# Kernel tuning notes

Measured on AMD Instinct MI355X. Metric: run time of the kernel, lower is better.

## Reference

```python
import jax, jax.numpy as jnp
import numpy as np

TEMP = 0.07
MOMENTUM = 0.2
K = 8192          # number of sampled negatives per row
NUM_CLASSES = 1000
B, N, D = 256, 32768, 2048
NEG_INF = -1e30


def _gumbel(key, shape):
    u = jax.random.uniform(key, shape, minval=1e-6, maxval=1.0)
    return -jnp.log(-jnp.log(u))


def setup_inputs() -> dict:
    key = jax.random.key(0)
    k1, k2, k3, k4, k5 = jax.random.split(key, 5)
    f = jax.random.normal(k1, (B, D), dtype=jnp.float32)
    f_nv = jax.random.normal(k2, (B, D), dtype=jnp.float32)
    # warmed-up memory bank (the real module L2-normalizes rows on update)
    features = jax.random.normal(k3, (N, D), dtype=jnp.float32)
    features = features / jnp.linalg.norm(features, axis=1, keepdims=True)
    labels = jax.random.randint(k4, (N,), 0, NUM_CLASSES)
    indexes = jax.random.randint(k5, (B,), 0, N)
    return {"f": f, "f_nv": f_nv, "features": features,
            "labels": labels, "indexes": indexes}


def reference(f, f_nv, features, labels, indexes):
    rkey = jax.random.key(42)
    kg1, kg2, kg3 = jax.random.split(rkey, 3)
    k = features                                   # [N, D] memory bank snapshot
    bsz = f.shape[0]

    # l_pos = <f_nv_i, k[indexes_i]>
    l_pos = jnp.sum(f_nv * k[indexes], axis=1, keepdims=True)   # [B, 1]

    mat = jnp.matmul(f, k.T)                       # [B, N]
    mat_sim = jnp.matmul(f_nv, k.T)                # [B, N]

    batch_labels = labels[indexes]                 # [B]
    pos_mask = labels[None, :] == batch_labels[:, None]         # [B, N]

    # torch.randperm-based sampling -> vectorized masked Gumbel sampling.
    # argmax of gumbel restricted to mask = uniform draw from masked set;
    # top-K of gumbel restricted to complement = K draws w/o replacement.
    g1 = _gumbel(kg1, (bsz, k.shape[0]))
    g2 = _gumbel(kg2, (bsz, k.shape[0]))
    g3 = _gumbel(kg3, (bsz, k.shape[0]))

    pos_idx_wogan = jnp.argmax(jnp.where(pos_mask, g1, NEG_INF), axis=1)
    positives_wogan = jnp.take_along_axis(mat, pos_idx_wogan[:, None], axis=1)  # [B,1]

    pos_idx = jnp.argmax(jnp.where(pos_mask, g2, NEG_INF), axis=1)
    positives = jnp.take_along_axis(mat_sim, pos_idx[:, None], axis=1)          # [B,1]

    _, neg_idx = jax.lax.top_k(jnp.where(pos_mask, NEG_INF, g3), K)             # [B,K]
    negatives = jnp.take_along_axis(mat_sim, neg_idx, axis=1)                   # [B,K]

    def ce_target0(logits):
        # CrossEntropyLoss with all targets == 0
        return -jax.nn.log_softmax(logits, axis=1)[:, 0].mean()

    self_out = jnp.concatenate([l_pos, negatives], axis=1) / TEMP
    inter_out = jnp.concatenate([positives, negatives], axis=1) / TEMP
    inter_out_wogan = jnp.concatenate([positives_wogan, negatives], axis=1) / TEMP

    memory_loss = ce_target0(self_out) + ce_target0(inter_out) + ce_target0(inter_out_wogan)

    # no-grad momentum update of the bank (F.normalize uses eps=1e-12)
    upd = MOMENTUM * k[indexes] + (1.0 - MOMENTUM) * f
    upd = upd / jnp.maximum(jnp.linalg.norm(upd, axis=1, keepdims=True), 1e-12)
    new_features = jax.lax.stop_gradient(features.at[indexes].set(upd))

    return memory_loss, new_features
```

## Files before the change

kernel.cpp:

```cpp
#include <hip/hip_runtime.h>
#include <stdint.h>

#define TEMP      0.07f
#define BATCH     256
#define NROWS     32768
#define DIM       2048
#define KNEG      8192

typedef __attribute__((ext_vector_type(8))) short bf16x8;
typedef __attribute__((ext_vector_type(4))) float f32x4;

__host__ __device__ inline void tf2x32(uint32_t ka, uint32_t kb,
                                       uint32_t x0, uint32_t x1,
                                       uint32_t& o0, uint32_t& o1) {
  uint32_t ks2 = ka ^ kb ^ 0x1BD11BDAu;
#define TFR(r) { x0 += x1; x1 = (x1 << r) | (x1 >> (32 - r)); x1 ^= x0; }
  x0 += ka; x1 += kb;
  TFR(13) TFR(15) TFR(26) TFR(6)
  x0 += kb;  x1 += ks2 + 1u;
  TFR(17) TFR(29) TFR(16) TFR(24)
  x0 += ks2; x1 += ka + 2u;
  TFR(13) TFR(15) TFR(26) TFR(6)
  x0 += ka;  x1 += kb + 3u;
  TFR(17) TFR(29) TFR(16) TFR(24)
  x0 += kb;  x1 += ks2 + 4u;
  TFR(13) TFR(15) TFR(26) TFR(6)
  x0 += ks2; x1 += ka + 5u;
#undef TFR
  o0 = x0; o1 = x1;
}

__device__ inline uint32_t ubits_at(uint32_t ka, uint32_t kb, uint32_t q) {
  uint32_t a, b; tf2x32(ka, kb, 0u, q, a, b);
  return (a ^ b) >> 9;
}

__device__ inline float block_sum(float v, float* sm) {
  __syncthreads();
  const int lane = threadIdx.x & 63;
  const int w = threadIdx.x >> 6;
  const int nw = blockDim.x >> 6;
  for (int o = 32; o; o >>= 1) v += __shfl_down(v, o, 64);
  if (lane == 0) sm[w] = v;
  __syncthreads();
  if (w == 0) {
    float x = (lane < nw) ? sm[lane] : 0.f;
    for (int o = 8; o; o >>= 1) x += __shfl_down(x, o, 64);
    if (lane == 0) sm[0] = x;
  }
  __syncthreads();
  return sm[0];
}

#define BM 256
#define BN 128
#define BK 64
#define NT (DIM / BK)

__device__ inline uint32_t pk2(float a, float b) {
  uint32_t ua = __float_as_uint(a), ub = __float_as_uint(b);
  ua = (ua + 0x7FFFu + ((ua >> 16) & 1u)) >> 16;
  ub = (ub + 0x7FFFu + ((ub >> 16) & 1u)) >> 16;
  return ua | (ub << 16);
}

__global__ __launch_bounds__(512, 2) void gemm_fused(
    const float* __restrict__ A,
    const float* __restrict__ B,
    float* __restrict__ C,
    float* __restrict__ outF,
    int copy_skip_rows) {
  __shared__ short As[2][BM * BK];
  __shared__ short Bs[2][BN * BK];
  const int t = threadIdx.x;
  const int bn = blockIdx.x;
  const int lane = t & 63, wave = t >> 6;
  const int wr = wave >> 2, wc = wave & 3;
  const int ld_row = t >> 4;
  const int ld_c4 = t & 15;

  float4 ra[8], rb[4];
  f32x4 acc[8][2] = {};

#define LOADT(k0)                                                              \
  {                                                                            \
    _Pragma("unroll")                                                          \
    for (int s = 0; s < 8; ++s)                                                \
      ra[s] = *(const float4*)&A[(size_t)(ld_row + 32 * s) * DIM + (k0) + ld_c4 * 4]; \
    _Pragma("unroll")                                                          \
    for (int s = 0; s < 4; ++s)                                                \
      rb[s] = *(const float4*)&B[(size_t)(bn * BN + ld_row + 32 * s) * DIM + (k0) + ld_c4 * 4]; \
  }

#define WRITET(buf, k0)                                                        \
  {                                                                            \
    _Pragma("unroll")                                                          \
    for (int s = 0; s < 8; ++s) {                                              \
      int r = ld_row + 32 * s;                                                 \
      uint32_t off = (uint32_t)r * (BK * 2) +                                  \
                     (((uint32_t)ld_c4 * 8) ^ (((uint32_t)r & 7u) << 4));      \
      *(uint2*)((char*)As[buf] + off) =                                        \
          make_uint2(pk2(ra[s].x, ra[s].y), pk2(ra[s].z, ra[s].w));            \
    }                                                                          \
    _Pragma("unroll")                                                          \
    for (int s = 0; s < 4; ++s) {                                              \
      int r = ld_row + 32 * s;                                                 \
      uint32_t off = (uint32_t)r * (BK * 2) +                                  \
                     (((uint32_t)ld_c4 * 8) ^ (((uint32_t)r & 7u) << 4));      \
      *(uint2*)((char*)Bs[buf] + off) =                                        \
          make_uint2(pk2(rb[s].x, rb[s].y), pk2(rb[s].z, rb[s].w));            \
      int g = bn * BN + r;                                                     \
      if (g >= copy_skip_rows) {                                               \
        float* d = &outF[(size_t)g * DIM + (k0) + ld_c4 * 4];                  \
        d[0] = rb[s].x; d[1] = rb[s].y; d[2] = rb[s].z; d[3] = rb[s].w;        \
      }                                                                        \
    }                                                                          \
  }

#define COMPUTET(buf)                                                          \
  {                                                                            \
    _Pragma("unroll")                                                          \
    for (int kk = 0; kk < 2; ++kk) {                                           \
      bf16x8 af[8], bfr[2];                                                    \
      const uint32_t kb = (uint32_t)(kk * 64 + ((lane >> 4) << 4));            \
      _Pragma("unroll")                                                        \
      for (int m = 0; m < 8; ++m) {                                            \
        uint32_t rr = (uint32_t)(wr * 128 + m * 16 + (lane & 15));             \
        af[m] = *(const bf16x8*)((const char*)As[buf] + rr * (BK * 2) +        \
                                 (kb ^ ((rr & 7u) << 4)));                     \
      }                                                                        \
      _Pragma("unroll")                                                        \
      for (int n = 0; n < 2; ++n) {                                            \
        uint32_t rr = (uint32_t)(wc * 32 + n * 16 + (lane & 15));              \
        bfr[n] = *(const bf16x8*)((const char*)Bs[buf] + rr * (BK * 2) +       \
                                  (kb ^ ((rr & 7u) << 4)));                    \
      }                                                                        \
      _Pragma("unroll")                                                        \
      for (int m = 0; m < 8; ++m)                                              \
        _Pragma("unroll")                                                      \
        for (int n = 0; n < 2; ++n)                                            \
          acc[m][n] = __builtin_amdgcn_mfma_f32_16x16x32_bf16(                 \
              af[m], bfr[n], acc[m][n], 0, 0, 0);                              \
    }                                                                          \
  }

  LOADT(0);
  WRITET(0, 0);
  __syncthreads();
  for (int t0 = 0; t0 < NT; ++t0) {
    if (t0 + 1 < NT) LOADT((t0 + 1) * BK);
    COMPUTET(t0 & 1);
    if (t0 + 1 < NT) {
      WRITET((t0 + 1) & 1, (t0 + 1) * BK);
      __syncthreads();
    }
  }

  const int col_l = lane & 15, rg = (lane >> 4) * 4;
#pragma unroll
  for (int m = 0; m < 8; ++m)
#pragma unroll
    for (int n = 0; n < 2; ++n) {
      size_t base = (size_t)(wr * 128 + m * 16 + rg) * NROWS
                  + (size_t)(bn * BN + wc * 32 + n * 16 + col_l);
#pragma unroll
      for (int r = 0; r < 4; ++r)
        C[base + (size_t)r * NROWS] = acc[m][n][r];
    }
#undef LOADT
#undef WRITET
#undef COMPUTET
}

__global__ __launch_bounds__(1024) void sample_loss(
    const float* __restrict__ f, const float* __restrict__ f_nv,
    const float* __restrict__ features, const int* __restrict__ labels,
    const int* __restrict__ indexes, const float* __restrict__ mat_sim,
    float* __restrict__ row_loss,
    uint32_t k1a, uint32_t k1b, uint32_t k2a, uint32_t k2b,
    uint32_t k3a, uint32_t k3b) {
  __shared__ uint32_t keys[NROWS];
  __shared__ uint32_t hist4[4][256];
  __shared__ uint32_t hist[256];
  __shared__ unsigned long long am1, am2;
  __shared__ int tie_j[128];
  __shared__ int tie_cnt;
  __shared__ float sred[16];
  __shared__ float swm[16], sws[16];
  __shared__ uint32_t bc_prefix, bc_rem;
  __shared__ int blab_s;

  const int t = threadIdx.x;
  const int i = blockIdx.x;
  const size_t mbase = (size_t)i * NROWS;

  if (t == 0) {
    blab_s = labels[indexes[i]];
    am1 = 0ull; am2 = 0ull; tie_cnt = 0;
  }
  __syncthreads();
  const int blab = blab_s;

#pragma unroll 2
  for (int s = 0; s < NROWS / 1024; ++s) {
    int j = t + 1024 * s;
    uint32_t q = (uint32_t)i * NROWS + (uint32_t)j;
    int lab = labels[j];
    if (lab == blab) {
      keys[j] = 0u;
      unsigned long long lo = (unsigned long long)(uint32_t)(NROWS - 1 - j);
      uint32_t u1 = ubits_at(k1a, k1b, q);
      uint32_t u2 = ubits_at(k2a, k2b, q);
      atomicMax(&am1, ((unsigned long long)u1 << 32) | lo);
      atomicMax(&am2, ((unsigned long long)u2 << 32) | lo);
    } else {
      keys[j] = ubits_at(k3a, k3b, q);
    }
  }
  __syncthreads();

  const int jw = NROWS - 1 - (int)(unsigned)(am1 & 0xFFFFFFFFull);
  const int jp = NROWS - 1 - (int)(unsigned)(am2 & 0xFFFFFFFFull);

  const int bank = indexes[i];
  float d1 = 0.f, d2 = 0.f, d3 = 0.f;
  for (int d = t; d < DIM; d += 1024) {
    float fnv = f_nv[(size_t)i * DIM + d];
    d1 += fnv * features[(size_t)bank * DIM + d];
    d2 += f[(size_t)i * DIM + d] * features[(size_t)jw * DIM + d];
    d3 += fnv * features[(size_t)jp * DIM + d];
  }
  const float l_pos = block_sum(d1, sred);
  const float posw  = block_sum(d2, sred);
  const float posv  = block_sum(d3, sred);

  uint32_t prefix = 0, remaining = KNEG;
  const int shifts[3] = {15, 7, 0};
  const int nbits[3]  = {8, 8, 7};
  for (int p = 0; p < 3; ++p) {
    const int sh = shifts[p];
    const int nb = 1 << nbits[p];
    ((uint32_t*)hist4)[t] = 0u;
    __syncthreads();
    const int hsel = t >> 8;
    for (int s = 0; s < NROWS / 1024; ++s) {
      int j = t + 1024 * s;
      uint32_t k = keys[j];
      bool ok = (p == 0) || ((k >> (sh + nbits[p])) == prefix);
      if (ok) atomicAdd(&hist4[hsel][(k >> sh) & (uint32_t)(nb - 1)], 1u);
    }
    __syncthreads();
    if (t < nb) hist[t] = hist4[0][t] + hist4[1][t] + hist4[2][t] + hist4[3][t];
    __syncthreads();
    if (t == 0) {
      uint32_t c = 0; int b = nb - 1;
      for (;; --b) {
        c += hist[b];
        if (c >= remaining || b == 0) break;
      }
      bc_prefix = (prefix << nbits[p]) | (uint32_t)b;
      bc_rem = remaining - (c - hist[b]);
    }
    __syncthreads();
    prefix = bc_prefix; remaining = bc_rem;
  }
  const uint32_t T = prefix;
  const uint32_t need = remaining;

  float m = -INFINITY, ssum = 0.f;
  for (int s = 0; s < NROWS / 1024; ++s) {
    int j = t + 1024 * s;
    uint32_t k = keys[j];
    if (k > T) {
      float v = mat_sim[mbase + j] / TEMP;
      if (v <= m) ssum += expf(v - m);
      else { ssum = ssum * expf(m - v) + 1.0f; m = v; }
    } else if (k == T) {
      int p = atomicAdd(&tie_cnt, 1);
      if (p < 128) tie_j[p] = j;
    }
  }
  for (int o = 32; o; o >>= 1) {
    float m2 = __shfl_down(m, o, 64);
    float s2 = __shfl_down(ssum, o, 64);
    if (m2 > m) { ssum = ssum * expf(m - m2) + s2; m = m2; }
    else if (m2 != -INFINITY) ssum += s2 * expf(m2 - m);
  }
  if ((t & 63) == 0) { swm[t >> 6] = m; sws[t >> 6] = ssum; }
  __syncthreads();
  if (t < 64) {
    float mm = (t < 16) ? swm[t] : -INFINITY;
    float ss = (t < 16) ? sws[t] : 0.f;
    for (int o = 8; o; o >>= 1) {
      float m2 = __shfl_down(mm, o, 64);
      float s2 = __shfl_down(ss, o, 64);
      if (m2 > mm) { ss = ss * expf(mm - m2) + s2; mm = m2; }
      else if (m2 != -INFINITY) ss += s2 * expf(m2 - mm);
    }
    if (t == 0) { swm[0] = mm; sws[0] = ss; }
  }
  __syncthreads();

  if (t == 0) {
    float M = swm[0], S = sws[0];
    int tc = tie_cnt;
    if (tc <= 128) {
      for (int a2 = 1; a2 < tc; ++a2) {
        int v = tie_j[a2]; int b2 = a2 - 1;
        while (b2 >= 0 && tie_j[b2] > v) { tie_j[b2 + 1] = tie_j[b2]; --b2; }
        tie_j[b2 + 1] = v;
      }
      for (uint32_t r = 0; r < need; ++r) {
        float v = mat_sim[mbase + tie_j[r]] / TEMP;
        if (v <= M) S += expf(v - M);
        else { S = S * expf(M - v) + 1.0f; M = v; }
      }
    } else {
      uint32_t taken = 0;
      for (int j = 0; j < NROWS && taken < need; ++j) {
        if (keys[j] == T) {
          float v = mat_sim[mbase + j] / TEMP;
          if (v <= M) S += expf(v - M);
          else { S = S * expf(M - v) + 1.0f; M = v; }
          ++taken;
        }
      }
    }
    float lp = l_pos / TEMP, pv = posv / TEMP, pw = posw / TEMP;
    float L = 0.f;
    { float X = fmaxf(M, lp); L += X + logf(expf(lp - X) + S * expf(M - X)) - lp; }
    { float X = fmaxf(M, pv); L += X + logf(expf(pv - X) + S * expf(M - X)) - pv; }
    { float X = fmaxf(M, pw); L += X + logf(expf(pw - X) + S * expf(M - X)) - pw; }
    row_loss[i] = L;
  }
}

__global__ void finalize_loss(const float* __restrict__ row_loss,
                              float* __restrict__ out) {
  __shared__ float sm[4];
  int t = threadIdx.x;
  float v = row_loss[t];
  for (int o = 32; o; o >>= 1) v += __shfl_down(v, o, 64);
  if ((t & 63) == 0) sm[t >> 6] = v;
  __syncthreads();
  if (t == 0) out[0] = (sm[0] + sm[1] + sm[2] + sm[3]) * (1.0f / BATCH);
}

__global__ void copy_front(const float* __restrict__ src,
                           float* __restrict__ dst, int n4) {
  int idx = blockIdx.x * blockDim.x + threadIdx.x;
  int stride = gridDim.x * blockDim.x;
  for (int i = idx; i < n4; i += stride) {
    float4 v = *(const float4*)&src[(size_t)i * 4];
    float* d = &dst[(size_t)i * 4];
    d[0] = v.x; d[1] = v.y; d[2] = v.z; d[3] = v.w;
  }
}

__global__ __launch_bounds__(256) void update_rows(
    const float* __restrict__ f, const float* __restrict__ features,
    const int* __restrict__ indexes, float* __restrict__ outF) {
  __shared__ float sred[16];
  const int i = blockIdx.x;
  const int row = indexes[i];
  for (int i2 = i + 1; i2 < BATCH; ++i2)
    if (indexes[i2] == row) return;
  const int t = threadIdx.x;
  float ss = 0.f;
  for (int d = t; d < DIM; d += 256) {
    float u = 0.2f * features[(size_t)row * DIM + d] + 0.8f * f[(size_t)i * DIM + d];
    ss += u * u;
  }
  ss = block_sum(ss, sred);
  float nrm = fmaxf(sqrtf(ss), 1e-12f);
  for (int d = t; d < DIM; d += 256) {
    float u = 0.2f * features[(size_t)row * DIM + d] + 0.8f * f[(size_t)i * DIM + d];
    outF[(size_t)row * DIM + d] = u / nrm;
  }
}

extern "C" void kernel_launch(void* const* d_in, const int* in_sizes, int n_in,
                              void* d_out, int out_size, void* d_ws, size_t ws_size,
                              hipStream_t stream) {
  (void)in_sizes; (void)n_in; (void)out_size;
  const float* f        = (const float*)d_in[0];
  const float* f_nv     = (const float*)d_in[1];
  const float* features = (const float*)d_in[2];
  const int*   labels   = (const int*)d_in[3];
  const int*   indexes  = (const int*)d_in[4];
  float* out = (float*)d_out;

  const size_t need = ((size_t)BATCH * NROWS + 256) * sizeof(float);
  float* mat_sim;
  float* row_loss;
  int skip_rows;
  bool use_ws = (d_ws != nullptr) && (ws_size >= need);
  if (use_ws) {
    mat_sim = (float*)d_ws;
    row_loss = mat_sim + (size_t)BATCH * NROWS;
    skip_rows = 0;
  } else {
    mat_sim = out + 4;
    row_loss = out + 4 + (size_t)BATCH * NROWS;
    skip_rows = 4224;
  }

  uint32_t c[6];
  { uint32_t a, b;
    tf2x32(0u, 42u, 0u, 0u, a, b); c[0] = a; c[1] = b;
    tf2x32(0u, 42u, 0u, 1u, a, b); c[2] = a; c[3] = b;
    tf2x32(0u, 42u, 0u, 2u, a, b); c[4] = a; c[5] = b; }

  gemm_fused<<<dim3(NROWS / BN), dim3(512), 0, stream>>>(
      f_nv, features, mat_sim, out + 1, skip_rows);
  sample_loss<<<dim3(BATCH), dim3(1024), 0, stream>>>(
      f, f_nv, features, labels, indexes, mat_sim, row_loss,
      c[0], c[1], c[2], c[3], c[4], c[5]);
  finalize_loss<<<dim3(1), dim3(256), 0, stream>>>(row_loss, out);
  if (!use_ws) {
    copy_front<<<dim3(2048), dim3(256), 0, stream>>>(
        features, out + 1, 4224 * DIM / 4);
  }
  update_rows<<<dim3(BATCH), dim3(256), 0, stream>>>(f, features, indexes, out + 1);
}
```

Measured before the change: 289.0 us.

## Pre-convert A to MFMA-fragment bf16 layout and shrink GEMM column tiles

A new kernel converts f_nv to bf16 once and stores it in the exact per-lane MFMA fragment order. The GEMM then reads A fragments straight from global memory (mostly cache hits) and keeps only B in shared memory. Column tiles shrink from 128 to 32 with 256 threads, which raises the block count and occupancy. The aim is to remove the redundant per-block fp32-to-bf16 conversion and LDS staging of A. In exchange, A fragments are re-read from L2 by every block, and the fallback path moves the copy skip boundary to make room for the new buffer.

After: 299.4 us. 1.04x slower.

```diff
diff --git a/kernel.cpp b/kernel.cpp
--- a/kernel.cpp
+++ b/kernel.cpp
@@ -52,11 +52,6 @@
   return sm[0];
 }
 
-#define BM 256
-#define BN 128
-#define BK 64
-#define NT (DIM / BK)
-
 __device__ inline uint32_t pk2(float a, float b) {
   uint32_t ua = __float_as_uint(a), ub = __float_as_uint(b);
   ua = (ua + 0x7FFFu + ((ua >> 16) & 1u)) >> 16;
@@ -64,112 +59,105 @@
   return ua | (ub << 16);
 }
 
-__global__ __launch_bounds__(512, 2) void gemm_fused(
-    const float* __restrict__ A,
+__global__ __launch_bounds__(256) void cvtA(const float* __restrict__ A,
+                                            uint32_t* __restrict__ Abf) {
+  const int t = threadIdx.x;
+  const int w = blockIdx.x * 4 + (t >> 6);
+  const int l = t & 63;
+  const int mt = w >> 6, kt = w & 63;
+  const float* src = &A[(size_t)(mt * 16 + (l & 15)) * DIM + kt * 32 + (l >> 4) * 8];
+  float4 f0 = *(const float4*)src;
+  float4 f1 = *(const float4*)(src + 4);
+  *(uint4*)(Abf + (size_t)w * 256 + l * 4) =
+      make_uint4(pk2(f0.x, f0.y), pk2(f0.z, f0.w), pk2(f1.x, f1.y), pk2(f1.z, f1.w));
+}
+
+#define BN2 32
+#define BK2 64
+#define NT2 (DIM / BK2)
+
+__global__ __launch_bounds__(256, 4) void gemm_fused(
+    const uint32_t* __restrict__ Abf,
     const float* __restrict__ B,
     float* __restrict__ C,
     float* __restrict__ outF,
-    int copy_skip_rows) {
-  __shared__ short As[2][BM * BK];
-  __shared__ short Bs[2][BN * BK];
+    int skip) {
+  __shared__ uint32_t Bs[2][BN2 * BK2 / 2];
   const int t = threadIdx.x;
   const int bn = blockIdx.x;
-  const int lane = t & 63, wave = t >> 6;
-  const int wr = wave >> 2, wc = wave & 3;
-  const int ld_row = t >> 4;
-  const int ld_c4 = t & 15;
-
-  float4 ra[8], rb[4];
-  f32x4 acc[8][2] = {};
-
-#define LOADT(k0)                                                              \
-  {                                                                            \
-    _Pragma("unroll")                                                          \
-    for (int s = 0; s < 8; ++s)                                                \
-      ra[s] = *(const float4*)&A[(size_t)(ld_row + 32 * s) * DIM + (k0) + ld_c4 * 4]; \
-    _Pragma("unroll")                                                          \
-    for (int s = 0; s < 4; ++s)                                                \
-      rb[s] = *(const float4*)&B[(size_t)(bn * BN + ld_row + 32 * s) * DIM + (k0) + ld_c4 * 4]; \
-  }
-
-#define WRITET(buf, k0)                                                        \
-  {                                                                            \
-    _Pragma("unroll")                                                          \
-    for (int s = 0; s < 8; ++s) {                                              \
-      int r = ld_row + 32 * s;                                                 \
-      uint32_t off = (uint32_t)r * (BK * 2) +                                  \
-                     (((uint32_t)ld_c4 * 8) ^ (((uint32_t)r & 7u) << 4));      \
-      *(uint2*)((char*)As[buf] + off) =                                        \
-          make_uint2(pk2(ra[s].x, ra[s].y), pk2(ra[s].z, ra[s].w));            \
-    }                                                                          \
-    _Pragma("unroll")                                                          \
-    for (int s = 0; s < 4; ++s) {                                              \
-      int r = ld_row + 32 * s;                                                 \
-      uint32_t off = (uint32_t)r * (BK * 2) +                                  \
-                     (((uint32_t)ld_c4 * 8) ^ (((uint32_t)r & 7u) << 4));      \
-      *(uint2*)((char*)Bs[buf] + off) =                                        \
-          make_uint2(pk2(rb[s].x, rb[s].y), pk2(rb[s].z, rb[s].w));            \
-      int g = bn * BN + r;                                                     \
-      if (g >= copy_skip_rows) {                                               \
-        float* d = &outF[(size_t)g * DIM + (k0) + ld_c4 * 4];                  \
-        d[0] = rb[s].x; d[1] = rb[s].y; d[2] = rb[s].z; d[3] = rb[s].w;        \
-      }                                                                        \
-    }                                                                          \
-  }
-
-#define COMPUTET(buf)                                                          \
-  {                                                                            \
+  const int l = t & 63, w = t >> 6;
+  const int sr = t >> 3, sg = t & 7;
+  const size_t srcRow = (size_t)(bn * BN2 + sr) * DIM;
+  const int swslot = (sr * 32) + ((sg ^ (sr & 7)) * 4);
+
+  float4 b0, b1;
+  f32x4 acc[4][2] = {};
+
+#define SLOAD(k0) {                                                            \
+    b0 = *(const float4*)&B[srcRow + (k0) + sg * 8];                           \
+    b1 = *(const float4*)&B[srcRow + (k0) + sg * 8 + 4]; }
+
+#define SWRITE(buf) {                                                          \
+    *(uint4*)&Bs[buf][swslot] = make_uint4(pk2(b0.x, b0.y), pk2(b0.z, b0.w),   \
+                                           pk2(b1.x, b1.y), pk2(b1.z, b1.w)); }
+
+#define SOUT(k0) {                                                             \
+    int g = bn * BN2 + sr;                                                     \
+    if (g >= skip) {                                                           \
+      float* d = &outF[(size_t)g * DIM + (k0) + sg * 8];                       \
+      d[0] = b0.x; d[1] = b0.y; d[2] = b0.z; d[3] = b0.w;                      \
+      d[4] = b1.x; d[5] = b1.y; d[6] = b1.z; d[7] = b1.w; } }
+
+#define COMPUTE(buf, t0) {                                                     \
     _Pragma("unroll")                                                          \
     for (int kk = 0; kk < 2; ++kk) {                                           \
-      bf16x8 af[8], bfr[2];                                                    \
-      const uint32_t kb = (uint32_t)(kk * 64 + ((lane >> 4) << 4));            \
+      bf16x8 af[4];                                                            \
       _Pragma("unroll")                                                        \
-      for (int m = 0; m < 8; ++m) {                                            \
-        uint32_t rr = (uint32_t)(wr * 128 + m * 16 + (lane & 15));             \
-        af[m] = *(const bf16x8*)((const char*)As[buf] + rr * (BK * 2) +        \
-                                 (kb ^ ((rr & 7u) << 4)));                     \
+      for (int m = 0; m < 4; ++m) {                                            \
+        int mt = w * 4 + m;                                                    \
+        af[m] = *(const bf16x8*)(Abf +                                         \
+                 ((size_t)(mt * 64 + ((t0) * 2 + kk)) * 64 + l) * 4);          \
+      }                                                                        \
+      bf16x8 bfr[2];                                                           \
+      _Pragma("unroll")                                                        \
+      for (int n = 0; n < 2; ++n) {                                            \
+        int r = n * 16 + (l & 15);                                             \
+        int slot = (kk * 4 + (l >> 4)) ^ (r & 7);                              \
+        bfr[n] = *(const bf16x8*)&Bs[buf][r * 32 + slot * 4];                  \
       }                                                                        \
       _Pragma("unroll")                                                        \
-      for (int n = 0; n < 2; ++n) {                                            \
-        uint32_t rr = (uint32_t)(wc * 32 + n * 16 + (lane & 15));              \
-        bfr[n] = *(const bf16x8*)((const char*)Bs[buf] + rr * (BK * 2) +       \
-                                  (kb ^ ((rr & 7u) << 4)));                    \
-      }                                                                        \
-      _Pragma("unroll")                                                        \
-      for (int m = 0; m < 8; ++m)                                              \
+      for (int m = 0; m < 4; ++m)                                              \
         _Pragma("unroll")                                                      \
         for (int n = 0; n < 2; ++n)                                            \
           acc[m][n] = __builtin_amdgcn_mfma_f32_16x16x32_bf16(                 \
               af[m], bfr[n], acc[m][n], 0, 0, 0);                              \
-    }                                                                          \
-  }
-
-  LOADT(0);
-  WRITET(0, 0);
-  __syncthreads();
-  for (int t0 = 0; t0 < NT; ++t0) {
-    if (t0 + 1 < NT) LOADT((t0 + 1) * BK);
-    COMPUTET(t0 & 1);
-    if (t0 + 1 < NT) {
-      WRITET((t0 + 1) & 1, (t0 + 1) * BK);
-      __syncthreads();
-    }
-  }
-
-  const int col_l = lane & 15, rg = (lane >> 4) * 4;
+    } }
+
+  SLOAD(0); SWRITE(0); SOUT(0);
+  __syncthreads();
+  for (int t0 = 0; t0 < NT2; ++t0) {
+    const int cur = t0 & 1;
+    if (t0 + 1 < NT2) SLOAD((t0 + 1) * BK2);
+    __builtin_amdgcn_sched_barrier(0);
+    COMPUTE(cur, t0);
+    if (t0 + 1 < NT2) { SWRITE(1 - cur); SOUT((t0 + 1) * BK2); }
+    __syncthreads();
+  }
+
+  const int colb = bn * BN2 + (l & 15);
 #pragma unroll
-  for (int m = 0; m < 8; ++m)
+  for (int m = 0; m < 4; ++m)
 #pragma unroll
     for (int n = 0; n < 2; ++n) {
-      size_t base = (size_t)(wr * 128 + m * 16 + rg) * NROWS
-                  + (size_t)(bn * BN + wc * 32 + n * 16 + col_l);
+      size_t base = (size_t)(w * 64 + m * 16 + (l >> 4) * 4) * NROWS + colb + n * 16;
 #pragma unroll
       for (int r = 0; r < 4; ++r)
         C[base + (size_t)r * NROWS] = acc[m][n][r];
     }
-#undef LOADT
-#undef WRITET
-#undef COMPUTET
+#undef SLOAD
+#undef SWRITE
+#undef SOUT
+#undef COMPUTE
 }
 
 __global__ __launch_bounds__(1024) void sample_loss(
@@ -390,19 +378,22 @@
   const int*   indexes  = (const int*)d_in[4];
   float* out = (float*)d_out;
 
-  const size_t need = ((size_t)BATCH * NROWS + 256) * sizeof(float);
+  const size_t need = ((size_t)BATCH * NROWS + 256 + 262144) * sizeof(float);
   float* mat_sim;
   float* row_loss;
+  uint32_t* Abf;
   int skip_rows;
   bool use_ws = (d_ws != nullptr) && (ws_size >= need);
   if (use_ws) {
     mat_sim = (float*)d_ws;
     row_loss = mat_sim + (size_t)BATCH * NROWS;
+    Abf = (uint32_t*)(row_loss + 256);
     skip_rows = 0;
   } else {
     mat_sim = out + 4;
-    row_loss = out + 4 + (size_t)BATCH * NROWS;
-    skip_rows = 4224;
+    row_loss = mat_sim + (size_t)BATCH * NROWS;
+    Abf = (uint32_t*)(row_loss + 256);
+    skip_rows = 4352;
   }
 
   uint32_t c[6];
@@ -411,15 +402,16 @@
     tf2x32(0u, 42u, 0u, 1u, a, b); c[2] = a; c[3] = b;
     tf2x32(0u, 42u, 0u, 2u, a, b); c[4] = a; c[5] = b; }
 
-  gemm_fused<<<dim3(NROWS / BN), dim3(512), 0, stream>>>(
-      f_nv, features, mat_sim, out + 1, skip_rows);
+  cvtA<<<dim3(256), dim3(256), 0, stream>>>(f_nv, Abf);
+  gemm_fused<<<dim3(NROWS / BN2), dim3(256), 0, stream>>>(
+      Abf, features, mat_sim, out + 1, skip_rows);
   sample_loss<<<dim3(BATCH), dim3(1024), 0, stream>>>(
       f, f_nv, features, labels, indexes, mat_sim, row_loss,
       c[0], c[1], c[2], c[3], c[4], c[5]);
   finalize_loss<<<dim3(1), dim3(256), 0, stream>>>(row_loss, out);
   if (!use_ws) {
     copy_front<<<dim3(2048), dim3(256), 0, stream>>>(
-        features, out + 1, 4224 * DIM / 4);
+        features, out + 1, 4352 * DIM / 4);
   }
   update_rows<<<dim3(BATCH), dim3(256), 0, stream>>>(f, features, indexes, out + 1);
 }
```
